# Optimization experiments

Measured on AMD Instinct MI355X. Metric: run time of the kernel, lower is better.

The kernel has to match this reference:

```python
import jax, jax.numpy as jnp
import numpy as np

N = 50000        # nodes
E = 1_600_000    # edges (avg degree 32)
F_IN = 128       # node feature dim
H = 64           # hidden_channels
C = 19           # output classes
G = 512          # graphs in the batch


def setup_inputs() -> dict:
    key = jax.random.key(0)
    ks = jax.random.split(key, 9)
    x = jax.random.normal(ks[0], (N, F_IN), dtype=jnp.float32)
    edge_index = jax.random.randint(ks[1], (2, E), 0, N, dtype=jnp.int64)
    batch = jnp.sort(jax.random.randint(ks[2], (N,), 0, G, dtype=jnp.int64))
    W1 = jax.random.normal(ks[3], (F_IN, H), dtype=jnp.float32) / np.sqrt(F_IN)
    b1 = jnp.zeros((H,), dtype=jnp.float32)
    W2 = jax.random.normal(ks[4], (H, H), dtype=jnp.float32) / np.sqrt(H)
    b2 = jnp.zeros((H,), dtype=jnp.float32)
    W_out = jax.random.normal(ks[5], (H, C), dtype=jnp.float32) / np.sqrt(H)
    b_out = jnp.zeros((C,), dtype=jnp.float32)
    return {"x": x, "edge_index": edge_index, "batch": batch,
            "W1": W1, "b1": b1, "W2": W2, "b2": b2,
            "W_out": W_out, "b_out": b_out}


def _gcn_conv(x, src, dst, W, b, n_nodes):
    """PyG GCNConv: add self-loops, symmetric D^-1/2 (A+I) D^-1/2 norm,
    linear transform first, gather-scale-scatter aggregation, then bias."""
    x = x @ W  # [N, out]
    loop = jnp.arange(n_nodes, dtype=src.dtype)
    s = jnp.concatenate([src, loop])  # source (message origin)
    d = jnp.concatenate([dst, loop])  # target (aggregation site)
    deg = jax.ops.segment_sum(jnp.ones_like(d, dtype=x.dtype), d,
                              num_segments=n_nodes)
    dinv = jnp.where(deg > 0, jax.lax.rsqrt(deg), 0.0)
    norm = dinv[s] * dinv[d]                       # [E+N]
    msg = x[s] * norm[:, None]                     # gather + scale
    out = jax.ops.segment_sum(msg, d, num_segments=n_nodes)  # scatter-add
    return out + b


def reference(x, edge_index, batch, W1, b1, W2, b2, W_out, b_out):
    src, dst = edge_index[0], edge_index[1]
    h = _gcn_conv(x, src, dst, W1, b1, N)
    h = jax.nn.relu(h)
    # F.dropout(training=False) -> identity (eval mode)
    h = _gcn_conv(h, src, dst, W2, b2, N)
    # global mean pool over graphs
    sums = jax.ops.segment_sum(h, batch, num_segments=G)        # [G, H]
    cnts = jax.ops.segment_sum(jnp.ones((N,), h.dtype), batch,
                               num_segments=G)                  # [G]
    pooled = sums / jnp.maximum(cnts, 1.0)[:, None]
    return pooled @ W_out + b_out                               # [G, C]
```

## Files before the change

kernel.cpp:

```cpp
#include <hip/hip_runtime.h>
#include <hip/hip_bf16.h>

#define F_IN 128
#define HID  64
#define NCLS 19
#define BW   128
#define NBMAX 512
#define ACAP 3072
#define BKCAP 5120
#define W1STR 136
#define W2STR 72

typedef __bf16 bf16x8 __attribute__((ext_vector_type(8)));
typedef float  f32x4  __attribute__((ext_vector_type(4)));

__device__ __forceinline__ float ldf(const void* p, long i, int fp32) {
    if (fp32) return ((const float*)p)[i];
    return __bfloat162float(((const __hip_bfloat16*)p)[i]);
}
__device__ __forceinline__ int ldi(const void* p, long i, int i64) {
    if (i64) return (int)((const long long*)p)[i];
    return ((const int*)p)[i];
}
__device__ __forceinline__ unsigned short f2bf(float f) {
    __hip_bfloat16 h = __float2bfloat16(f);
    unsigned short r;
    __builtin_memcpy(&r, &h, 2);
    return r;
}
__device__ __forceinline__ float bflo(unsigned u) { return __uint_as_float(u << 16); }
__device__ __forceinline__ float bfhi(unsigned u) { return __uint_as_float(u & 0xffff0000u); }

__device__ __forceinline__ bf16x8 ldfrag(const unsigned short* p) {
    uint4 u = *(const uint4*)p;
    return __builtin_bit_cast(bf16x8, u);
}
__device__ __forceinline__ bf16x8 ldfrag_any(const void* p, long off, int fp32) {
    if (!fp32) return ldfrag((const unsigned short*)p + off);
    const float4* f = (const float4*)((const float*)p + off);
    float4 u0 = f[0];
    float4 u1 = f[1];
    uint4 u = make_uint4((unsigned)f2bf(u0.x) | ((unsigned)f2bf(u0.y) << 16),
                         (unsigned)f2bf(u0.z) | ((unsigned)f2bf(u0.w) << 16),
                         (unsigned)f2bf(u1.x) | ((unsigned)f2bf(u1.y) << 16),
                         (unsigned)f2bf(u1.z) | ((unsigned)f2bf(u1.w) << 16));
    return __builtin_bit_cast(bf16x8, u);
}

__global__ __launch_bounds__(512) void k_detect(const void* x, const void* ei, int* flags,
                                                int* __restrict__ bcur, int NB) {
    int t = threadIdx.x;
    for (int b = t; b < NB; b += 512) bcur[b] = b * BKCAP;
    if (t != 0) return;
    const unsigned* xw = (const unsigned*)x;
    int bf16 = 1;
    for (int i = 0; i < 16; ++i) {
        unsigned w = xw[i];
        int elo = (w >> 7) & 0xFF;
        int ehi = (w >> 23) & 0xFF;
        if (elo < 100 || elo > 140 || ehi < 100 || ehi > 140) bf16 = 0;
    }
    const unsigned* iw = (const unsigned*)ei;
    int i64 = 1; unsigned anyev = 0;
    for (int k = 0; k < 8; ++k) {
        if (iw[2 * k + 1] != 0) i64 = 0;
        anyev |= iw[2 * k];
    }
    if (anyev == 0) i64 = 0;
    flags[0] = bf16 ? 0 : 1;
    flags[1] = i64;
}

__global__ __launch_bounds__(256) void k_bounds(const void* __restrict__ batch, int N, int G,
                                                int* __restrict__ bounds,
                                                const int* __restrict__ flags) {
    int i64 = flags[1];
    int i = blockIdx.x * 256 + threadIdx.x;
    if (i >= N) return;
    int b = min(max(ldi(batch, i, i64), 0), G - 1);
    int p = (i == 0) ? -1 : min(max(ldi(batch, (long)i - 1, i64), 0), G - 1);
    for (int g = p + 1; g <= b; ++g) bounds[g] = i;
    if (i == N - 1)
        for (int g = b + 1; g <= G; ++g) bounds[g] = N;
}

__global__ __launch_bounds__(512) void k_sortA(const void* __restrict__ ei, int E, int nbuck,
                                               int* bcur, int* __restrict__ bkt,
                                               const int* __restrict__ flags) {
    __shared__ int lbuf[ACAP];
    __shared__ unsigned short lbkt[ACAP];
    __shared__ int lh[NBMAX];
    __shared__ int lsc[NBMAX];
    __shared__ int lcur[NBMAX];
    __shared__ int gbase[NBMAX];
    __shared__ int wpart[8];
    int i64 = flags[1];
    int t = threadIdx.x;
    int e0 = blockIdx.x * ACAP;
    int e1 = min(E, e0 + ACAP);
    int cnt = e1 - e0;
    lh[t] = 0;
    __syncthreads();
    for (int e = e0 + t; e < e1; e += 512)
        atomicAdd(&lh[(ldi(ei, (long)E + e, i64) >> 7) & (NBMAX - 1)], 1);
    __syncthreads();
    int v = lh[t];
    int lane = t & 63, wq = t >> 6;
    int incl = v;
#pragma unroll
    for (int off = 1; off < 64; off <<= 1) {
        int n = __shfl_up(incl, off);
        if (lane >= off) incl += n;
    }
    if (lane == 63) wpart[wq] = incl;
    __syncthreads();
    if (t == 0) {
        int acc = 0;
#pragma unroll
        for (int i = 0; i < 8; ++i) { int xx = wpart[i]; wpart[i] = acc; acc += xx; }
    }
    __syncthreads();
    int ex = wpart[wq] + incl - v;
    lsc[t] = ex;
    lcur[t] = ex;
    gbase[t] = (v && t < nbuck) ? atomicAdd(&bcur[t], v) : 0;
    __syncthreads();
    for (int e = e0 + t; e < e1; e += 512) {
        int s = ldi(ei, e, i64);
        int d = ldi(ei, (long)E + e, i64);
        int b = (d >> 7) & (NBMAX - 1);
        int r = atomicAdd(&lcur[b], 1);
        r = min(max(r, 0), ACAP - 1);
        lbuf[r] = (s << 7) | (d & (BW - 1));
        lbkt[r] = (unsigned short)b;
    }
    __syncthreads();
    for (int i = t; i < cnt; i += 512) {
        int lo = lbkt[i];
        int idx = gbase[lo] + (i - lsc[lo]);
        if (idx >= lo * BKCAP && idx < (lo + 1) * BKCAP) bkt[idx] = lbuf[i];
    }
}

__global__ __launch_bounds__(512) void k_sortB(const int* __restrict__ bkt,
                                               const int* __restrict__ bcur,
                                               int N,
                                               int* __restrict__ csr,
                                               int* __restrict__ cursor,
                                               int* __restrict__ deg,
                                               float* __restrict__ dinv) {
    __shared__ int lstage[BKCAP];
    __shared__ int lcsr[BKCAP];
    __shared__ int lh[BW], lsc[BW], lcur[BW];
    int b = blockIdx.x, t = threadIdx.x;
    int base = b * BKCAP;
    int cnt = min(max(bcur[b] - base, 0), BKCAP);
    if (t < BW) lh[t] = 0;
    __syncthreads();
    for (int i = t; i < cnt; i += 512) {
        int w = __builtin_nontemporal_load(&bkt[base + i]);
        lstage[i] = w;
        atomicAdd(&lh[w & (BW - 1)], 1);
    }
    __syncthreads();
    if (t < BW) lsc[t] = lh[t];
    __syncthreads();
    for (int off = 1; off < BW; off <<= 1) {
        int a = (t < BW && t >= off) ? lsc[t - off] : 0;
        __syncthreads();
        if (t < BW) lsc[t] += a;
        __syncthreads();
    }
    if (t < BW) {
        int ex = lsc[t] - lh[t];
        lcur[t] = ex;
        int n = b * BW + t;
        if (n < N) {
            cursor[n] = base + ex;
            deg[n] = lh[t];
            dinv[n] = rsqrtf((float)(lh[t] + 1));
        }
    }
    __syncthreads();
    for (int i = t; i < cnt; i += 512) {
        int w = lstage[i];
        int r = atomicAdd(&lcur[w & (BW - 1)], 1);
        int sv = (int)((unsigned)w >> 7);
        if (sv >= N) sv = 0;
        r = min(max(r, 0), BKCAP - 1);
        lcsr[r] = sv;
    }
    __syncthreads();
    for (int i = t; i < cnt; i += 512) csr[base + i] = lcsr[i];
}

__global__ __launch_bounds__(256) void k_gemm1(const void* __restrict__ x,
                                               const void* __restrict__ W,
                                               const float* __restrict__ dinv,
                                               unsigned short* __restrict__ t, int N,
                                               const int* __restrict__ flags) {
    __shared__ __align__(16) unsigned short wt[HID * W1STR];
    int fp32 = flags[0];
    int tid = threadIdx.x;
    if (fp32) {
        const float* wf = (const float*)W;
        for (int i = tid * 4; i < F_IN * HID; i += 1024) {
            float4 w4 = *(const float4*)(wf + i);
            int k = i >> 6, n = i & 63;
            wt[(n + 0) * W1STR + k] = f2bf(w4.x);
            wt[(n + 1) * W1STR + k] = f2bf(w4.y);
            wt[(n + 2) * W1STR + k] = f2bf(w4.z);
            wt[(n + 3) * W1STR + k] = f2bf(w4.w);
        }
    } else {
        for (int i = tid; i < F_IN * HID; i += 256) {
            int k = i >> 6, n = i & 63;
            wt[n * W1STR + k] = f2bf(ldf(W, i, 0));
        }
    }
    __syncthreads();
    int wv = tid >> 6, lane = tid & 63;
    int quad = lane >> 4, l16 = lane & 15;
    int r0 = blockIdx.x * 64 + wv * 16;
    int rowA = min(r0 + l16, N - 1);
    bf16x8 a[4];
#pragma unroll
    for (int kq = 0; kq < 4; ++kq)
        a[kq] = ldfrag_any(x, (long)rowA * F_IN + kq * 32 + quad * 8, fp32);
    float di[4];
    int rowC = r0 + quad * 4;
#pragma unroll
    for (int r = 0; r < 4; ++r) di[r] = (rowC + r < N) ? dinv[rowC + r] : 0.f;
#pragma unroll
    for (int cg = 0; cg < 4; ++cg) {
        int col = cg * 16 + l16;
        f32x4 acc = {0.f, 0.f, 0.f, 0.f};
#pragma unroll
        for (int kq = 0; kq < 4; ++kq) {
            bf16x8 b = ldfrag(wt + col * W1STR + kq * 32 + quad * 8);
            acc = __builtin_amdgcn_mfma_f32_16x16x32_bf16(a[kq], b, acc, 0, 0, 0);
        }
#pragma unroll
        for (int r = 0; r < 4; ++r) {
            int row = rowC + r;
            if (row < N) t[(size_t)row * HID + col] = f2bf(di[r] * acc[r]);
        }
    }
}

__global__ __launch_bounds__(256) void k_gemm2(const unsigned short* __restrict__ h,
                                               const void* __restrict__ W,
                                               const float* __restrict__ dinv,
                                               unsigned short* __restrict__ t, int N,
                                               const int* __restrict__ flags) {
    __shared__ __align__(16) unsigned short wt[HID * W2STR];
    int fp32 = flags[0];
    int tid = threadIdx.x;
    if (fp32) {
        const float* wf = (const float*)W;
        for (int i = tid * 4; i < HID * HID; i += 1024) {
            float4 w4 = *(const float4*)(wf + i);
            int k = i >> 6, n = i & 63;
            wt[(n + 0) * W2STR + k] = f2bf(w4.x);
            wt[(n + 1) * W2STR + k] = f2bf(w4.y);
            wt[(n + 2) * W2STR + k] = f2bf(w4.z);
            wt[(n + 3) * W2STR + k] = f2bf(w4.w);
        }
    } else {
        for (int i = tid; i < HID * HID; i += 256) {
            int k = i >> 6, n = i & 63;
            wt[n * W2STR + k] = f2bf(ldf(W, i, 0));
        }
    }
    __syncthreads();
    int wv = tid >> 6, lane = tid & 63;
    int quad = lane >> 4, l16 = lane & 15;
    int r0 = blockIdx.x * 64 + wv * 16;
    int rowA = min(r0 + l16, N - 1);
    bf16x8 a[2];
#pragma unroll
    for (int kq = 0; kq < 2; ++kq)
        a[kq] = ldfrag(h + (size_t)rowA * HID + kq * 32 + quad * 8);
    float di[4];
    int rowC = r0 + quad * 4;
#pragma unroll
    for (int r = 0; r < 4; ++r) di[r] = (rowC + r < N) ? dinv[rowC + r] : 0.f;
#pragma unroll
    for (int cg = 0; cg < 4; ++cg) {
        int col = cg * 16 + l16;
        f32x4 acc = {0.f, 0.f, 0.f, 0.f};
#pragma unroll
        for (int kq = 0; kq < 2; ++kq) {
            bf16x8 b = ldfrag(wt + col * W2STR + kq * 32 + quad * 8);
            acc = __builtin_amdgcn_mfma_f32_16x16x32_bf16(a[kq], b, acc, 0, 0, 0);
        }
#pragma unroll
        for (int r = 0; r < 4; ++r) {
            int row = rowC + r;
            if (row < N) t[(size_t)row * HID + col] = f2bf(di[r] * acc[r]);
        }
    }
}

template <bool RELU>
__global__ __launch_bounds__(256) void k_agg(const unsigned short* __restrict__ t,
                                             const int* __restrict__ csr,
                                             const int* __restrict__ cursor,
                                             const int* __restrict__ deg,
                                             const float* __restrict__ dinv,
                                             const void* __restrict__ bias,
                                             unsigned short* __restrict__ out,
                                             int N, int SZ, const int* __restrict__ flags) {
    __shared__ float sbias[HID];
    __shared__ int scur[8];
    __shared__ int sdeg[8];
    __shared__ float sdv[8];
    int tid = threadIdx.x;
    int nb = blockIdx.x * 8;
    if (tid < HID) sbias[tid] = ldf(bias, tid, flags[0]);
    if (tid >= 64 && tid < 72) {
        int q = tid - 64;
        int node = nb + q;
        int c = 0, d = 0;
        float dv = 0.f;
        if (node < N) { c = cursor[node]; d = deg[node]; dv = dinv[node]; }
        scur[q] = c; sdeg[q] = d; sdv[q] = dv;
    }
    __syncthreads();
    int wv = tid >> 6, lane = tid & 63;
    int half = lane >> 5;
    int idx = wv * 2 + half;
    int node = nb + idx;
    int l = lane & 31;
    int g = l >> 3;
    int l8 = (l & 7) * 8;
    bool alive = (node < N);
    int snode = alive ? node : 0;
    int beg = scur[idx];
    int dg = sdeg[idx];
    beg = min(max(beg, 0), SZ);
    int end = beg + min(max(dg, 0), SZ - beg);
    uint4 sv = make_uint4(0u, 0u, 0u, 0u);
    if (g == 0) sv = *(const uint4*)(t + (size_t)snode * HID + l8);
    f32x4 A = {0.f, 0.f, 0.f, 0.f};
    f32x4 B = {0.f, 0.f, 0.f, 0.f};
    int e = beg;
    for (; e + 32 <= end; e += 32) {
        int s[8];
#pragma unroll
        for (int k = 0; k < 8; ++k) {
            int si = __builtin_nontemporal_load(&csr[e + 4 * k + g]);
            s[k] = ((unsigned)si < (unsigned)N) ? si : 0;
        }
        uint4 v[8];
#pragma unroll
        for (int k = 0; k < 8; ++k)
            v[k] = *(const uint4*)(t + (size_t)s[k] * HID + l8);
#pragma unroll
        for (int k = 0; k < 8; ++k) {
            f32x4 lo = {bflo(v[k].x), bfhi(v[k].x), bflo(v[k].y), bfhi(v[k].y)};
            f32x4 hi = {bflo(v[k].z), bfhi(v[k].z), bflo(v[k].w), bfhi(v[k].w)};
            A += lo;
            B += hi;
        }
    }
    if (e < end) {
        int s[8];
#pragma unroll
        for (int k = 0; k < 8; ++k) {
            int i = e + 4 * k + g;
            int si = __builtin_nontemporal_load(&csr[i < end ? i : end - 1]);
            s[k] = ((unsigned)si < (unsigned)N) ? si : 0;
        }
        uint4 v[8];
#pragma unroll
        for (int k = 0; k < 8; ++k)
            v[k] = *(const uint4*)(t + (size_t)s[k] * HID + l8);
#pragma unroll
        for (int k = 0; k < 8; ++k) {
            if (e + 4 * k + g < end) {
                f32x4 lo = {bflo(v[k].x), bfhi(v[k].x), bflo(v[k].y), bfhi(v[k].y)};
                f32x4 hi = {bflo(v[k].z), bfhi(v[k].z), bflo(v[k].w), bfhi(v[k].w)};
                A += lo;
                B += hi;
            }
        }
    }
#pragma unroll
    for (int m = 8; m <= 16; m <<= 1) {
#pragma unroll
        for (int c = 0; c < 4; ++c) {
            A[c] += __shfl_xor(A[c], m);
            B[c] += __shfl_xor(B[c], m);
        }
    }
    if (g == 0 && alive) {
        f32x4 slo = {bflo(sv.x), bfhi(sv.x), bflo(sv.y), bfhi(sv.y)};
        f32x4 shi = {bflo(sv.z), bfhi(sv.z), bflo(sv.w), bfhi(sv.w)};
        A += slo;
        B += shi;
        float di = sdv[idx];
        float v0 = di * A[0] + sbias[l8 + 0];
        float v1 = di * A[1] + sbias[l8 + 1];
        float v2 = di * A[2] + sbias[l8 + 2];
        float v3 = di * A[3] + sbias[l8 + 3];
        float v4 = di * B[0] + sbias[l8 + 4];
        float v5 = di * B[1] + sbias[l8 + 5];
        float v6 = di * B[2] + sbias[l8 + 6];
        float v7 = di * B[3] + sbias[l8 + 7];
        if (RELU) {
            v0 = fmaxf(v0, 0.f); v1 = fmaxf(v1, 0.f); v2 = fmaxf(v2, 0.f); v3 = fmaxf(v3, 0.f);
            v4 = fmaxf(v4, 0.f); v5 = fmaxf(v5, 0.f); v6 = fmaxf(v6, 0.f); v7 = fmaxf(v7, 0.f);
        }
        uint4 pk;
        pk.x = (unsigned)f2bf(v0) | ((unsigned)f2bf(v1) << 16);
        pk.y = (unsigned)f2bf(v2) | ((unsigned)f2bf(v3) << 16);
        pk.z = (unsigned)f2bf(v4) | ((unsigned)f2bf(v5) << 16);
        pk.w = (unsigned)f2bf(v6) | ((unsigned)f2bf(v7) << 16);
        *(uint4*)(out + (size_t)node * HID + l8) = pk;
    }
}

__global__ __launch_bounds__(256) void k_poolout(const unsigned short* __restrict__ h2,
                                                 const int* __restrict__ bounds, int N,
                                                 const void* __restrict__ Wout,
                                                 const void* __restrict__ bout,
                                                 void* __restrict__ out,
                                                 const int* __restrict__ flags) {
    __shared__ float pr[HID];
    __shared__ float sacc[4][HID];
    int g = blockIdx.x;
    int start = min(max(bounds[g], 0), N);
    int endg = min(max(bounds[g + 1], start), N);
    int tid = threadIdx.x;
    int wv = tid >> 6, lane = tid & 63;
    int half = lane >> 5;
    int l = lane & 31;
    float s0 = 0.f, s1 = 0.f;
    for (int r = start + wv * 2 + half; r < endg; r += 8) {
        unsigned u = *(const unsigned*)(h2 + (size_t)r * HID + 2 * l);
        s0 += bflo(u);
        s1 += bfhi(u);
    }
    s0 += __shfl_xor(s0, 32);
    s1 += __shfl_xor(s1, 32);
    if (lane < 32) {
        sacc[wv][2 * l] = s0;
        sacc[wv][2 * l + 1] = s1;
    }
    __syncthreads();
    if (tid < HID) {
        float inv = 1.f / fmaxf((float)(endg - start), 1.f);
        pr[tid] = (sacc[0][tid] + sacc[1][tid] + sacc[2][tid] + sacc[3][tid]) * inv;
    }
    __syncthreads();
    int fp32 = flags[0];
    if (tid < NCLS) {
        float acc = ldf(bout, tid, fp32);
#pragma unroll 4
        for (int k = 0; k < HID; ++k)
            acc += pr[k] * ldf(Wout, k * NCLS + tid, fp32);
        if (fp32) ((float*)out)[g * NCLS + tid] = acc;
        else ((__hip_bfloat16*)out)[g * NCLS + tid] = __float2bfloat16(acc);
    }
}

extern "C" void kernel_launch(void* const* d_in, const int* in_sizes, int n_in,
                              void* d_out, int out_size, void* d_ws, size_t ws_size,
                              hipStream_t stream) {
    const void* x    = d_in[0];
    const void* ei   = d_in[1];
    const void* bat  = d_in[2];
    const void* W1   = d_in[3];
    const void* b1   = d_in[4];
    const void* W2   = d_in[5];
    const void* b2   = d_in[6];
    const void* Wout = d_in[7];
    const void* bout = d_in[8];

    const int N = in_sizes[0] / F_IN;
    const int E = in_sizes[1] / 2;
    const int G = out_size / NCLS;
    const int NB = (N + BW - 1) / BW;
    const int SZ = NB * BKCAP;

    char* ws = (char*)d_ws;
    size_t off = 0;
    auto carve = [&](size_t bytes) -> void* {
        void* p = ws + off;
        off = (off + bytes + 255) & ~(size_t)255;
        return p;
    };
    int*            flags  = (int*)carve(64);
    int*            deg    = (int*)carve((size_t)N * 4);
    int*            cursor = (int*)carve((size_t)N * 4);
    float*          dinv   = (float*)carve((size_t)N * 4);
    int*            bcur   = (int*)carve((size_t)NB * 4);
    int*            bounds = (int*)carve((size_t)(G + 1) * 4);
    int*            csr    = (int*)carve((size_t)SZ * 4);
    int*            bkt    = (int*)carve((size_t)SZ * 4);
    unsigned short* t      = (unsigned short*)carve((size_t)N * HID * 2);
    unsigned short* h      = (unsigned short*)carve((size_t)N * HID * 2);
    (void)ws_size; (void)n_in;

    k_detect<<<1, 512, 0, stream>>>(x, ei, flags, bcur, NB);
    k_bounds<<<(N + 255) / 256, 256, 0, stream>>>(bat, N, G, bounds, flags);

    int na = (E + ACAP - 1) / ACAP;
    k_sortA<<<na, 512, 0, stream>>>(ei, E, NB, bcur, bkt, flags);
    k_sortB<<<NB, 512, 0, stream>>>(bkt, bcur, N, csr, cursor, deg, dinv);

    int gb = (N + 63) / 64;
    int ab = (N + 7) / 8;
    k_gemm1<<<gb, 256, 0, stream>>>(x, W1, dinv, t, N, flags);
    k_agg<true><<<ab, 256, 0, stream>>>(t, csr, cursor, deg, dinv, b1, h, N, SZ, flags);
    k_gemm2<<<gb, 256, 0, stream>>>(h, W2, dinv, t, N, flags);
    k_agg<false><<<ab, 256, 0, stream>>>(t, csr, cursor, deg, dinv, b2, h, N, SZ, flags);
    k_poolout<<<G, 256, 0, stream>>>(h, bounds, N, Wout, bout, d_out, flags);
}
```

Before: 207.5 us.

## Fuse layer-1 aggregation with layer-2 GEMM and register-cache dst in sortA

Merges the first GCN aggregation (gather, scale, bias, ReLU) with the second layer's 64x64 MFMA transform in one kernel. Each block aggregates 8 nodes into shared memory, then multiplies them by W2 there. This removes a kernel launch and the write and re-read of the intermediate h buffer. In exchange, each block redundantly loads and transposes W2 into LDS, and half of each 16-row MFMA tile is zero padding. Separately, sortA now keeps each edge's destination index in registers across both passes instead of reading it from global memory twice.

```diff
diff --git a/kernel.cpp b/kernel.cpp
--- a/kernel.cpp
+++ b/kernel.cpp
@@ -10,6 +10,7 @@
 #define BKCAP 5120
 #define W1STR 136
 #define W2STR 72
+#define HROWSTR 72
 
 typedef __bf16 bf16x8 __attribute__((ext_vector_type(8)));
 typedef float  f32x4  __attribute__((ext_vector_type(4)));
@@ -101,8 +102,15 @@
     int cnt = e1 - e0;
     lh[t] = 0;
     __syncthreads();
-    for (int e = e0 + t; e < e1; e += 512)
-        atomicAdd(&lh[(ldi(ei, (long)E + e, i64) >> 7) & (NBMAX - 1)], 1);
+    int dreg[6];
+#pragma unroll
+    for (int j = 0; j < 6; ++j) {
+        int e = e0 + t + 512 * j;
+        dreg[j] = (e < e1) ? ldi(ei, (long)E + e, i64) : -1;
+    }
+#pragma unroll
+    for (int j = 0; j < 6; ++j)
+        if (dreg[j] >= 0) atomicAdd(&lh[(dreg[j] >> 7) & (NBMAX - 1)], 1);
     __syncthreads();
     int v = lh[t];
     int lane = t & 63, wq = t >> 6;
@@ -125,13 +133,15 @@
     lcur[t] = ex;
     gbase[t] = (v && t < nbuck) ? atomicAdd(&bcur[t], v) : 0;
     __syncthreads();
-    for (int e = e0 + t; e < e1; e += 512) {
+#pragma unroll
+    for (int j = 0; j < 6; ++j) {
+        if (dreg[j] < 0) continue;
+        int e = e0 + t + 512 * j;
         int s = ldi(ei, e, i64);
-        int d = ldi(ei, (long)E + e, i64);
-        int b = (d >> 7) & (NBMAX - 1);
+        int b = (dreg[j] >> 7) & (NBMAX - 1);
         int r = atomicAdd(&lcur[b], 1);
         r = min(max(r, 0), ACAP - 1);
-        lbuf[r] = (s << 7) | (d & (BW - 1));
+        lbuf[r] = (s << 7) | (dreg[j] & (BW - 1));
         lbkt[r] = (unsigned short)b;
     }
     __syncthreads();
@@ -248,16 +258,37 @@
     }
 }
 
-__global__ __launch_bounds__(256) void k_gemm2(const unsigned short* __restrict__ h,
-                                               const void* __restrict__ W,
-                                               const float* __restrict__ dinv,
-                                               unsigned short* __restrict__ t, int N,
-                                               const int* __restrict__ flags) {
+__global__ __launch_bounds__(256) void k_agg1mm(const unsigned short* __restrict__ t,
+                                                const int* __restrict__ csr,
+                                                const int* __restrict__ cursor,
+                                                const int* __restrict__ deg,
+                                                const float* __restrict__ dinv,
+                                                const void* __restrict__ bias,
+                                                const void* __restrict__ W2,
+                                                unsigned short* __restrict__ out,
+                                                int N, int SZ, const int* __restrict__ flags) {
+    __shared__ float sbias[HID];
+    __shared__ int scur[8];
+    __shared__ int sdeg[8];
+    __shared__ float sdv[8];
     __shared__ __align__(16) unsigned short wt[HID * W2STR];
+    __shared__ __align__(16) unsigned short hrow[16][HROWSTR];
     int fp32 = flags[0];
     int tid = threadIdx.x;
+    int nb = blockIdx.x * 8;
+    if (tid < HID) sbias[tid] = ldf(bias, tid, fp32);
+    if (tid >= 64 && tid < 72) {
+        int q = tid - 64;
+        int node = nb + q;
+        int c = 0, d = 0;
+        float dv = 0.f;
+        if (node < N) { c = cursor[node]; d = deg[node]; dv = dinv[node]; }
+        scur[q] = c; sdeg[q] = d; sdv[q] = dv;
+    }
+    for (int i = tid; i < 8 * HROWSTR; i += 256)
+        hrow[8 + i / HROWSTR][i % HROWSTR] = 0;
     if (fp32) {
-        const float* wf = (const float*)W;
+        const float* wf = (const float*)W2;
         for (int i = tid * 4; i < HID * HID; i += 1024) {
             float4 w4 = *(const float4*)(wf + i);
             int k = i >> 6, n = i & 63;
@@ -267,37 +298,122 @@
             wt[(n + 3) * W2STR + k] = f2bf(w4.w);
         }
     } else {
+        const unsigned short* ws16 = (const unsigned short*)W2;
         for (int i = tid; i < HID * HID; i += 256) {
             int k = i >> 6, n = i & 63;
-            wt[n * W2STR + k] = f2bf(ldf(W, i, 0));
+            wt[n * W2STR + k] = ws16[i];
         }
     }
     __syncthreads();
     int wv = tid >> 6, lane = tid & 63;
-    int quad = lane >> 4, l16 = lane & 15;
-    int r0 = blockIdx.x * 64 + wv * 16;
-    int rowA = min(r0 + l16, N - 1);
-    bf16x8 a[2];
-#pragma unroll
-    for (int kq = 0; kq < 2; ++kq)
-        a[kq] = ldfrag(h + (size_t)rowA * HID + kq * 32 + quad * 8);
-    float di[4];
-    int rowC = r0 + quad * 4;
-#pragma unroll
-    for (int r = 0; r < 4; ++r) di[r] = (rowC + r < N) ? dinv[rowC + r] : 0.f;
-#pragma unroll
-    for (int cg = 0; cg < 4; ++cg) {
-        int col = cg * 16 + l16;
+    int half = lane >> 5;
+    int idx = wv * 2 + half;
+    int node = nb + idx;
+    int l = lane & 31;
+    int g = l >> 3;
+    int l8 = (l & 7) * 8;
+    bool alive = (node < N);
+    int snode = alive ? node : 0;
+    int beg = scur[idx];
+    int dg = sdeg[idx];
+    beg = min(max(beg, 0), SZ);
+    int end = beg + min(max(dg, 0), SZ - beg);
+    uint4 sv = make_uint4(0u, 0u, 0u, 0u);
+    if (g == 0) sv = *(const uint4*)(t + (size_t)snode * HID + l8);
+    f32x4 A = {0.f, 0.f, 0.f, 0.f};
+    f32x4 B = {0.f, 0.f, 0.f, 0.f};
+    int e = beg;
+    for (; e + 32 <= end; e += 32) {
+        int s[8];
+#pragma unroll
+        for (int k = 0; k < 8; ++k) {
+            int si = __builtin_nontemporal_load(&csr[e + 4 * k + g]);
+            s[k] = ((unsigned)si < (unsigned)N) ? si : 0;
+        }
+        uint4 v[8];
+#pragma unroll
+        for (int k = 0; k < 8; ++k)
+            v[k] = *(const uint4*)(t + (size_t)s[k] * HID + l8);
+#pragma unroll
+        for (int k = 0; k < 8; ++k) {
+            f32x4 lo = {bflo(v[k].x), bfhi(v[k].x), bflo(v[k].y), bfhi(v[k].y)};
+            f32x4 hi = {bflo(v[k].z), bfhi(v[k].z), bflo(v[k].w), bfhi(v[k].w)};
+            A += lo;
+            B += hi;
+        }
+    }
+    if (e < end) {
+        int s[8];
+#pragma unroll
+        for (int k = 0; k < 8; ++k) {
+            int i = e + 4 * k + g;
+            int si = __builtin_nontemporal_load(&csr[i < end ? i : end - 1]);
+            s[k] = ((unsigned)si < (unsigned)N) ? si : 0;
+        }
+        uint4 v[8];
+#pragma unroll
+        for (int k = 0; k < 8; ++k)
+            v[k] = *(const uint4*)(t + (size_t)s[k] * HID + l8);
+#pragma unroll
+        for (int k = 0; k < 8; ++k) {
+            if (e + 4 * k + g < end) {
+                f32x4 lo = {bflo(v[k].x), bfhi(v[k].x), bflo(v[k].y), bfhi(v[k].y)};
+                f32x4 hi = {bflo(v[k].z), bfhi(v[k].z), bflo(v[k].w), bfhi(v[k].w)};
+                A += lo;
+                B += hi;
+            }
+        }
+    }
+#pragma unroll
+    for (int m = 8; m <= 16; m <<= 1) {
+#pragma unroll
+        for (int c = 0; c < 4; ++c) {
+            A[c] += __shfl_xor(A[c], m);
+            B[c] += __shfl_xor(B[c], m);
+        }
+    }
+    if (g == 0) {
+        f32x4 slo = {bflo(sv.x), bfhi(sv.x), bflo(sv.y), bfhi(sv.y)};
+        f32x4 shi = {bflo(sv.z), bfhi(sv.z), bflo(sv.w), bfhi(sv.w)};
+        A += slo;
+        B += shi;
+        float di = sdv[idx];
+        float v0 = fmaxf(di * A[0] + sbias[l8 + 0], 0.f);
+        float v1 = fmaxf(di * A[1] + sbias[l8 + 1], 0.f);
+        float v2 = fmaxf(di * A[2] + sbias[l8 + 2], 0.f);
+        float v3 = fmaxf(di * A[3] + sbias[l8 + 3], 0.f);
+        float v4 = fmaxf(di * B[0] + sbias[l8 + 4], 0.f);
+        float v5 = fmaxf(di * B[1] + sbias[l8 + 5], 0.f);
+        float v6 = fmaxf(di * B[2] + sbias[l8 + 6], 0.f);
+        float v7 = fmaxf(di * B[3] + sbias[l8 + 7], 0.f);
+        uint4 pk;
+        pk.x = (unsigned)f2bf(v0) | ((unsigned)f2bf(v1) << 16);
+        pk.y = (unsigned)f2bf(v2) | ((unsigned)f2bf(v3) << 16);
+        pk.z = (unsigned)f2bf(v4) | ((unsigned)f2bf(v5) << 16);
+        pk.w = (unsigned)f2bf(v6) | ((unsigned)f2bf(v7) << 16);
+        *(uint4*)(&hrow[idx][l8]) = pk;
+    }
+    __syncthreads();
+    {
+        int quad = lane >> 4, l16 = lane & 15;
+        bf16x8 a2[2];
+#pragma unroll
+        for (int kq = 0; kq < 2; ++kq)
+            a2[kq] = ldfrag(&hrow[l16][kq * 32 + quad * 8]);
+        int col = wv * 16 + l16;
         f32x4 acc = {0.f, 0.f, 0.f, 0.f};
 #pragma unroll
         for (int kq = 0; kq < 2; ++kq) {
             bf16x8 b = ldfrag(wt + col * W2STR + kq * 32 + quad * 8);
-            acc = __builtin_amdgcn_mfma_f32_16x16x32_bf16(a[kq], b, acc, 0, 0, 0);
-        }
-#pragma unroll
-        for (int r = 0; r < 4; ++r) {
-            int row = rowC + r;
-            if (row < N) t[(size_t)row * HID + col] = f2bf(di[r] * acc[r]);
+            acc = __builtin_amdgcn_mfma_f32_16x16x32_bf16(a2[kq], b, acc, 0, 0, 0);
+        }
+        if (quad < 2) {
+#pragma unroll
+            for (int r = 0; r < 4; ++r) {
+                int row = quad * 4 + r;
+                int n2 = nb + row;
+                if (n2 < N) out[(size_t)n2 * HID + col] = f2bf(sdv[row] * acc[r]);
+            }
         }
     }
 }
@@ -513,8 +629,7 @@
     int gb = (N + 63) / 64;
     int ab = (N + 7) / 8;
     k_gemm1<<<gb, 256, 0, stream>>>(x, W1, dinv, t, N, flags);
-    k_agg<true><<<ab, 256, 0, stream>>>(t, csr, cursor, deg, dinv, b1, h, N, SZ, flags);
-    k_gemm2<<<gb, 256, 0, stream>>>(h, W2, dinv, t, N, flags);
-    k_agg<false><<<ab, 256, 0, stream>>>(t, csr, cursor, deg, dinv, b2, h, N, SZ, flags);
-    k_poolout<<<G, 256, 0, stream>>>(h, bounds, N, Wout, bout, d_out, flags);
-}
+    k_agg1mm<<<ab, 256, 0, stream>>>(t, csr, cursor, deg, dinv, b1, W2, h, N, SZ, flags);
+    k_agg<false><<<ab, 256, 0, stream>>>(h, csr, cursor, deg, dinv, b2, t, N, SZ, flags);
+    k_poolout<<<G, 256, 0, stream>>>(t, bounds, N, Wout, bout, d_out, flags);
+}
```

New measurement: 204.6 us. Within noise of the previous version (-1.4%).
